# Kernel optimization log

Hardware: AMD Instinct MI355X
Metric: run time of the kernel (lower is better)

The kernel has to match this reference:

```python
import jax, jax.numpy as jnp
import numpy as np

B, S, D = 8, 1024, 768
H = 12
HD = D // H  # 64
SCALE = 1.0 / (HD ** 0.5)


def setup_inputs() -> dict:
    key = jax.random.key(0)
    ks = jax.random.split(key, 5)
    x = jax.random.normal(ks[0], (B, S, D), dtype=jnp.float32)
    W_qkv = jax.random.normal(ks[1], (D, 3 * D), dtype=jnp.float32) * 0.02
    b_qkv = jax.random.normal(ks[2], (3 * D,), dtype=jnp.float32) * 0.02
    W_proj = jax.random.normal(ks[3], (D, D), dtype=jnp.float32) * 0.02
    b_proj = jax.random.normal(ks[4], (D,), dtype=jnp.float32) * 0.02
    return {"x": x, "W_qkv": W_qkv, "b_qkv": b_qkv, "W_proj": W_proj, "b_proj": b_proj}


def reference(x, W_qkv, b_qkv, W_proj, b_proj):
    b, s, d = x.shape
    # QKV projection: (B, S, 3D) -> (3, B, H, S, HD)
    qkv = x @ W_qkv + b_qkv
    qkv = qkv.reshape(b, s, 3, H, HD).transpose(2, 0, 3, 1, 4)
    q, k, v = qkv[0], qkv[1], qkv[2]
    # scaled dot-product attention (full matrix, as in the original)
    scores = jnp.einsum("bhqd,bhkd->bhqk", q, k) * SCALE
    attn = jax.nn.softmax(scores, axis=-1)
    out = jnp.einsum("bhqk,bhkd->bhqd", attn, v)
    # merge heads: (B, S, D)
    out = out.transpose(0, 2, 1, 3).reshape(b, s, d)
    return out @ W_proj + b_proj
```

## Files before the change

### kernel.cpp

```cpp
#include <hip/hip_runtime.h>
#include <math.h>

typedef __attribute__((ext_vector_type(8))) unsigned short ushortx8;
typedef __attribute__((ext_vector_type(8))) __bf16 bf16x8;
typedef __attribute__((ext_vector_type(4))) float floatx4;
typedef __attribute__((ext_vector_type(16))) float floatx16;

#define NH 12
#define SEQ 1024
#define DM 768
#define HD 64
#define GK 768
#define QK_SCALE 0.18033688011112042f

#define GLDS16(gp, lp) __builtin_amdgcn_global_load_lds( \
    (const __attribute__((address_space(1))) unsigned int*)(const void*)(gp), \
    (__attribute__((address_space(3))) unsigned int*)(lp), 16, 0, 0)

__device__ __forceinline__ unsigned short f2bf(float f) {
    union { float f; unsigned u; } v; v.f = f;
    unsigned r = v.u + 0x7fffu + ((v.u >> 16) & 1u);
    return (unsigned short)(r >> 16);
}

__device__ __forceinline__ unsigned pk2bf(float f0, float f1) {
    union { float f; unsigned u; } a, b; a.f = f0; b.f = f1;
    return ((a.u + 0x8000u) >> 16) | ((b.u + 0x8000u) & 0xffff0000u);
}

__device__ __forceinline__ float fast_exp2(float x) {
    float r;
    asm("v_exp_f32 %0, %1" : "=v"(r) : "v"(x));
    return r;
}

__global__ void k_prep(const float* __restrict__ x, unsigned short* __restrict__ x_bf,
                       const float* __restrict__ Wqkv, unsigned short* __restrict__ WqkvT,
                       const float* __restrict__ Wproj, unsigned short* __restrict__ WprojT) {
    __shared__ float tile[32][33];
    int bx = blockIdx.x;
    if (bx < 6144) {
        int i = bx * 256 + threadIdx.x;
        float4 v = ((const float4*)x)[i];
        ushort4 o;
        o.x = f2bf(v.x); o.y = f2bf(v.y); o.z = f2bf(v.z); o.w = f2bf(v.w);
        ((ushort4*)x_bf)[i] = o;
        return;
    }
    const float* in; unsigned short* out; int R, C, c0, r0;
    if (bx < 7872) {
        int t = bx - 6144;
        in = Wqkv; out = WqkvT; R = 768; C = 2304;
        c0 = (t % 72) * 32; r0 = (t / 72) * 32;
    } else {
        int t = bx - 7872;
        in = Wproj; out = WprojT; R = 768; C = 768;
        c0 = (t % 24) * 32; r0 = (t / 24) * 32;
    }
    int tx = threadIdx.x & 31, ty = threadIdx.x >> 5;
#pragma unroll
    for (int i = 0; i < 4; i++)
        tile[ty + 8 * i][tx] = in[(size_t)(r0 + ty + 8 * i) * C + c0 + tx];
    __syncthreads();
#pragma unroll
    for (int i = 0; i < 4; i++)
        out[(size_t)(c0 + ty + 8 * i) * R + r0 + tx] = f2bf(tile[tx][ty + 8 * i]);
}

__device__ __forceinline__ void stage6(const unsigned short* gA, const unsigned short* gB,
                                       unsigned short* lbuf, int w, int k0) {
#pragma unroll
    for (int g = 0; g < 4; g++)
        GLDS16(gA + (size_t)(w * 64 + g * 16) * GK + k0, lbuf + (w * 64 + g * 16) * 32);
#pragma unroll
    for (int g = 0; g < 2; g++)
        GLDS16(gB + (size_t)(w * 32 + g * 16) * GK + k0, lbuf + 8192 + (w * 32 + g * 16) * 32);
}

__device__ __forceinline__ void mfma24(const unsigned short* Ab, const unsigned short* Bb,
                                       int wm, int wn, int l15, int csw,
                                       floatx4 (&acc)[8][3]) {
    bf16x8 af[8], bfr[3];
#pragma unroll
    for (int m = 0; m < 8; m++)
        af[m] = __builtin_bit_cast(bf16x8,
            *(const ushortx8*)&Ab[(wm * 128 + m * 16 + l15) * 32 + csw]);
#pragma unroll
    for (int n = 0; n < 3; n++)
        bfr[n] = __builtin_bit_cast(bf16x8,
            *(const ushortx8*)&Bb[(wn * 48 + n * 16 + l15) * 32 + csw]);
#pragma unroll
    for (int m = 0; m < 8; m++)
#pragma unroll
        for (int n = 0; n < 3; n++)
            acc[m][n] = __builtin_amdgcn_mfma_f32_16x16x32_bf16(af[m], bfr[n], acc[m][n], 0, 0, 0);
}

__device__ __forceinline__ void gemm_mainloop(const unsigned short* __restrict__ A,
                                              const unsigned short* __restrict__ Bt,
                                              unsigned short* smem, int m0, int n0,
                                              int w, int lane, floatx4 (&acc)[8][3]) {
    int quad = lane >> 4, l15 = lane & 15;
    int wm = w >> 1, wn = w & 1;
    int rA = lane >> 2;
    int cSwz = ((lane & 3) ^ ((lane >> 3) & 3)) * 8;
    int csw = (quad ^ ((l15 >> 1) & 3)) * 8;
    const unsigned short* gA = A + (size_t)(m0 + rA) * GK + cSwz;
    const unsigned short* gB = Bt + (size_t)(n0 + rA) * GK + cSwz;

    stage6(gA, gB, smem, w, 0);
    stage6(gA, gB, smem + 12288, w, 32);
#pragma unroll 1
    for (int t = 0; t < 24; t++) {
        if (t < 23) asm volatile("s_waitcnt vmcnt(6)" ::: "memory");
        else        asm volatile("s_waitcnt vmcnt(0)" ::: "memory");
        __builtin_amdgcn_s_barrier();
        asm volatile("" ::: "memory");
        const unsigned short* Ab = smem + (t & 1) * 12288;
        __builtin_amdgcn_s_setprio(1);
        mfma24(Ab, Ab + 8192, wm, wn, l15, csw, acc);
        __builtin_amdgcn_s_setprio(0);
        asm volatile("" ::: "memory");
        __builtin_amdgcn_s_barrier();
        asm volatile("" ::: "memory");
        if (t < 22) stage6(gA, gB, smem + (t & 1) * 12288, w, (t + 2) * 32);
    }
}

__global__ __launch_bounds__(256, 3) void k_gemm_qkv(
    const unsigned short* __restrict__ A, const unsigned short* __restrict__ Bt,
    const float* __restrict__ bias,
    unsigned short* __restrict__ Qb, unsigned short* __restrict__ Kb,
    unsigned short* __restrict__ Vt) {
    __shared__ unsigned short smem[25344];
    int tid = threadIdx.x;
    int w = tid >> 6, lane = tid & 63;
    int quad = lane >> 4, l15 = lane & 15;
    int wm = w >> 1, wn = w & 1;
    int lin = blockIdx.x;
    int xcd = lin & 7, slot = lin >> 3;
    int mt_i = xcd * 4 + (slot & 3);
    int nt_i = slot >> 2;
    int m0 = mt_i * 256, n0 = nt_i * 96;

    floatx4 acc[8][3] = {};
    gemm_mainloop(A, Bt, smem, m0, n0, w, lane, acc);

    int tsel = nt_i / 8;
    int bb = m0 >> 10;
    int s_base0 = (m0 & 1023) + wm * 128;
    if (tsel < 2) {
        unsigned short* __restrict__ dst = (tsel == 0) ? Qb : Kb;
#pragma unroll
        for (int m = 0; m < 8; m++) {
            int s_base = s_base0 + m * 16 + quad * 4;
#pragma unroll
            for (int n = 0; n < 3; n++) {
                int n_g = n0 + wn * 48 + n * 16 + l15;
                int nloc = n_g - tsel * 768;
                int hh = nloc >> 6, dd = nloc & 63;
                float bv = bias[n_g];
                size_t base = ((size_t)(bb * NH + hh) * SEQ + s_base) * HD + dd;
                if (tsel == 0) {
#pragma unroll
                    for (int rg = 0; rg < 4; rg++)
                        dst[base + (size_t)rg * HD] = f2bf((acc[m][n][rg] + bv) * QK_SCALE);
                } else {
#pragma unroll
                    for (int rg = 0; rg < 4; rg++)
                        dst[base + (size_t)rg * HD] = f2bf(acc[m][n][rg] + bv);
                }
            }
        }
    } else {
        __syncthreads();
#pragma unroll
        for (int m = 0; m < 8; m++) {
#pragma unroll
            for (int n = 0; n < 3; n++) {
                int col = wn * 48 + n * 16 + l15;
                float bv = bias[n0 + col];
                ushort4 pk;
                pk.x = f2bf(acc[m][n][0] + bv);
                pk.y = f2bf(acc[m][n][1] + bv);
                pk.z = f2bf(acc[m][n][2] + bv);
                pk.w = f2bf(acc[m][n][3] + bv);
                *(ushort4*)&smem[col * 264 + wm * 128 + m * 16 + quad * 4] = pk;
            }
        }
        __syncthreads();
        if (tid < 192) {
            int col = tid >> 1, part = tid & 1;
            int dglob = (n0 - 1536) + col;
            int hh = dglob >> 6, dd = dglob & 63;
            size_t gbase = ((size_t)(bb * NH + hh) * HD + dd) * SEQ + (m0 & 1023) + part * 128;
#pragma unroll
            for (int i = 0; i < 16; i++)
                *(uint4*)&Vt[gbase + i * 8] = *(const uint4*)&smem[col * 264 + part * 128 + i * 8];
        }
    }
}

__global__ __launch_bounds__(256) void k_attn(
    const unsigned short* __restrict__ Qb, const unsigned short* __restrict__ Kb,
    const unsigned short* __restrict__ Vt, unsigned short* __restrict__ attn_out) {
    __shared__ unsigned short smem[16384];
    unsigned short* Ks = smem;
    unsigned short* Vts = smem + 8192;
    int tid = threadIdx.x;
    int w = tid >> 6, lane = tid & 63;
    int l31 = lane & 31, lh = lane >> 5;
    int lin = blockIdx.x;
    int xcd = lin & 7, slot = lin >> 3;
    int bh = xcd * 12 + (slot >> 3);
    int qt = slot & 7;
    int b = bh / NH, h = bh - b * NH;
    const unsigned short* Qp = Qb + (size_t)bh * SEQ * HD;
    const unsigned short* Kp = Kb + (size_t)bh * SEQ * HD;
    const unsigned short* Vp = Vt + (size_t)bh * HD * SEQ;
    int q0w = qt * 128 + w * 32;

    bf16x8 qf[4];
#pragma unroll
    for (int ds = 0; ds < 4; ds++)
        qf[ds] = __builtin_bit_cast(bf16x8,
            *(const ushortx8*)&Qp[(size_t)(q0w + l31) * HD + ds * 16 + lh * 8]);

    floatx16 o[2] = {};
    float lsum = 0.f;

    int rr = tid >> 3, cc8 = (tid & 7) * 8;
    int cs = cc8 ^ ((rr & 7) * 8);
    int rsw = (l31 & 7) * 8;

    {
        uint4 a = *(const uint4*)&Kp[(size_t)rr * HD + cc8];
        uint4 b2 = *(const uint4*)&Kp[(size_t)(rr + 32) * HD + cc8];
        uint4 c = *(const uint4*)&Vp[(size_t)rr * SEQ + cc8];
        uint4 d = *(const uint4*)&Vp[(size_t)(rr + 32) * SEQ + cc8];
        *(uint4*)&Ks[rr * 64 + cs] = a;
        *(uint4*)&Ks[(rr + 32) * 64 + cs] = b2;
        *(uint4*)&Vts[rr * 64 + cs] = c;
        *(uint4*)&Vts[(rr + 32) * 64 + cs] = d;
    }
    uint4 kr0 = *(const uint4*)&Kp[(size_t)(64 + rr) * HD + cc8];
    uint4 kr1 = *(const uint4*)&Kp[(size_t)(64 + rr + 32) * HD + cc8];
    uint4 vr0 = *(const uint4*)&Vp[(size_t)rr * SEQ + 64 + cc8];
    uint4 vr1 = *(const uint4*)&Vp[(size_t)(rr + 32) * SEQ + 64 + cc8];
    __syncthreads();

    for (int kb = 0; kb < SEQ; kb += 64) {
        int cur = (kb >> 6) & 1;
        if (kb + 64 < SEQ) {
            *(uint4*)&Ks[(cur ^ 1) * 4096 + rr * 64 + cs] = kr0;
            *(uint4*)&Ks[(cur ^ 1) * 4096 + (rr + 32) * 64 + cs] = kr1;
            *(uint4*)&Vts[(cur ^ 1) * 4096 + rr * 64 + cs] = vr0;
            *(uint4*)&Vts[(cur ^ 1) * 4096 + (rr + 32) * 64 + cs] = vr1;
            if (kb + 128 < SEQ) {
                kr0 = *(const uint4*)&Kp[(size_t)(kb + 128 + rr) * HD + cc8];
                kr1 = *(const uint4*)&Kp[(size_t)(kb + 128 + rr + 32) * HD + cc8];
                vr0 = *(const uint4*)&Vp[(size_t)rr * SEQ + kb + 128 + cc8];
                vr1 = *(const uint4*)&Vp[(size_t)(rr + 32) * SEQ + kb + 128 + cc8];
            }
        }

        floatx16 sc[2] = {};
        __builtin_amdgcn_s_setprio(1);
#pragma unroll
        for (int mt = 0; mt < 2; mt++)
#pragma unroll
            for (int ds = 0; ds < 4; ds++) {
                bf16x8 kf = __builtin_bit_cast(bf16x8,
                    *(const ushortx8*)&Ks[cur * 4096 + (mt * 32 + l31) * 64 + ((ds * 16 + lh * 8) ^ rsw)]);
                sc[mt] = __builtin_amdgcn_mfma_f32_32x32x16_bf16(kf, qf[ds], sc[mt], 0, 0, 0);
            }
        __builtin_amdgcn_s_setprio(0);

        float p0[16], p1[16];
#pragma unroll
        for (int r = 0; r < 16; r++) {
            p0[r] = fast_exp2(sc[0][r]);
            p1[r] = fast_exp2(sc[1][r]);
            lsum += p0[r] + p1[r];
        }

        uint4 pw[4];
#pragma unroll
        for (int mt = 0; mt < 2; mt++) {
            const float* pp = mt ? p1 : p0;
#pragma unroll
            for (int hf = 0; hf < 2; hf++) {
                unsigned a, bq, c, d;
                asm("v_cvt_pk_bf16_f32 %0, %1, %2" : "=v"(a)  : "v"(pp[hf * 8 + 0]), "v"(pp[hf * 8 + 1]));
                asm("v_cvt_pk_bf16_f32 %0, %1, %2" : "=v"(bq) : "v"(pp[hf * 8 + 4]), "v"(pp[hf * 8 + 5]));
                asm("v_cvt_pk_bf16_f32 %0, %1, %2" : "=v"(c)  : "v"(pp[hf * 8 + 2]), "v"(pp[hf * 8 + 3]));
                asm("v_cvt_pk_bf16_f32 %0, %1, %2" : "=v"(d)  : "v"(pp[hf * 8 + 6]), "v"(pp[hf * 8 + 7]));
                asm("v_permlane32_swap_b32 %0, %1" : "+v"(a), "+v"(bq));
                asm("v_permlane32_swap_b32 %0, %1" : "+v"(c), "+v"(d));
                uint4 wv; wv.x = a; wv.y = c; wv.z = bq; wv.w = d;
                pw[mt * 2 + hf] = wv;
            }
        }

        __builtin_amdgcn_s_setprio(1);
#pragma unroll
        for (int ks = 0; ks < 4; ks++) {
            bf16x8 pf = __builtin_bit_cast(bf16x8, pw[ks]);
#pragma unroll
            for (int mt = 0; mt < 2; mt++) {
                bf16x8 vf = __builtin_bit_cast(bf16x8,
                    *(const ushortx8*)&Vts[cur * 4096 + (mt * 32 + l31) * 64 + ((ks * 16 + lh * 8) ^ rsw)]);
                o[mt] = __builtin_amdgcn_mfma_f32_32x32x16_bf16(vf, pf, o[mt], 0, 0, 0);
            }
        }
        __builtin_amdgcn_s_setprio(0);

        __syncthreads();
    }

    lsum += __shfl_xor(lsum, 32, 64);
    float inv = 1.0f / lsum;

    unsigned short* Ptw = smem + w * 2304;
#pragma unroll
    for (int mt = 0; mt < 2; mt++)
#pragma unroll
        for (int g = 0; g < 4; g++) {
            uint2 pk;
            pk.x = pk2bf(o[mt][g * 4 + 0] * inv, o[mt][g * 4 + 1] * inv);
            pk.y = pk2bf(o[mt][g * 4 + 2] * inv, o[mt][g * 4 + 3] * inv);
            *(uint2*)&Ptw[l31 * 72 + mt * 32 + g * 8 + lh * 4] = pk;
        }
    __builtin_amdgcn_s_barrier();
#pragma unroll
    for (int pass = 0; pass < 4; pass++) {
        int row = pass * 8 + (lane >> 3);
        int col8 = (lane & 7) * 8;
        uint4 vv = *(const uint4*)&Ptw[row * 72 + col8];
        *(uint4*)&attn_out[(size_t)(b * SEQ + q0w + row) * DM + h * HD + col8] = vv;
    }
}

__device__ __forceinline__ void stage4(const unsigned short* gA, const unsigned short* gB,
                                       unsigned short* lbuf, int w, int k0) {
#pragma unroll
    for (int g = 0; g < 2; g++)
        GLDS16(gA + (size_t)(w * 32 + g * 16) * GK + k0, lbuf + (w * 32 + g * 16) * 32);
#pragma unroll
    for (int g = 0; g < 2; g++)
        GLDS16(gB + (size_t)(w * 32 + g * 16) * GK + k0, lbuf + 4096 + (w * 32 + g * 16) * 32);
}

__device__ __forceinline__ void mfma12(const unsigned short* Ab, const unsigned short* Bb,
                                       int wm, int wn, int l15, int csw,
                                       floatx4 (&acc)[4][3]) {
    bf16x8 af[4], bfr[3];
#pragma unroll
    for (int m = 0; m < 4; m++)
        af[m] = __builtin_bit_cast(bf16x8,
            *(const ushortx8*)&Ab[(wm * 64 + m * 16 + l15) * 32 + csw]);
#pragma unroll
    for (int n = 0; n < 3; n++)
        bfr[n] = __builtin_bit_cast(bf16x8,
            *(const ushortx8*)&Bb[(wn * 48 + n * 16 + l15) * 32 + csw]);
#pragma unroll
    for (int m = 0; m < 4; m++)
#pragma unroll
        for (int n = 0; n < 3; n++)
            acc[m][n] = __builtin_amdgcn_mfma_f32_16x16x32_bf16(af[m], bfr[n], acc[m][n], 0, 0, 0);
}

__global__ __launch_bounds__(256, 2) void k_gemm_proj(
    const unsigned short* __restrict__ A, const unsigned short* __restrict__ Bt,
    const float* __restrict__ bias, float* __restrict__ out) {
    __shared__ unsigned short smem[16384];
    int tid = threadIdx.x;
    int w = tid >> 6, lane = tid & 63;
    int quad = lane >> 4, l15 = lane & 15;
    int wm = w >> 1, wn = w & 1;
    int lin = blockIdx.x;
    int xcd = lin & 7, slot = lin >> 3;
    int mt_i = xcd * 8 + (slot & 7);
    int nt_i = slot >> 3;
    int m0 = mt_i * 128, n0 = nt_i * 96;

    int rA = lane >> 2;
    int cSwz = ((lane & 3) ^ ((lane >> 3) & 3)) * 8;
    int csw = (quad ^ ((l15 >> 1) & 3)) * 8;
    const unsigned short* gA = A + (size_t)(m0 + rA) * GK + cSwz;
    const unsigned short* gB = Bt + (size_t)(n0 + rA) * GK + cSwz;

    floatx4 acc[4][3] = {};
    stage4(gA, gB, smem, w, 0);
    stage4(gA, gB, smem + 8192, w, 32);
#pragma unroll 1
    for (int t = 0; t < 24; t++) {
        if (t < 23) asm volatile("s_waitcnt vmcnt(4)" ::: "memory");
        else        asm volatile("s_waitcnt vmcnt(0)" ::: "memory");
        __builtin_amdgcn_s_barrier();
        asm volatile("" ::: "memory");
        const unsigned short* Ab = smem + (t & 1) * 8192;
        __builtin_amdgcn_s_setprio(1);
        mfma12(Ab, Ab + 4096, wm, wn, l15, csw, acc);
        __builtin_amdgcn_s_setprio(0);
        asm volatile("" ::: "memory");
        __builtin_amdgcn_s_barrier();
        asm volatile("" ::: "memory");
        if (t < 22) stage4(gA, gB, smem + (t & 1) * 8192, w, (t + 2) * 32);
    }

#pragma unroll
    for (int m = 0; m < 4; m++) {
        int m_base = m0 + wm * 64 + m * 16 + quad * 4;
#pragma unroll
        for (int n = 0; n < 3; n++) {
            int n_g = n0 + wn * 48 + n * 16 + l15;
            float bv = bias[n_g];
#pragma unroll
            for (int rg = 0; rg < 4; rg++)
                out[(size_t)(m_base + rg) * DM + n_g] = acc[m][n][rg] + bv;
        }
    }
}

extern "C" void kernel_launch(void* const* d_in, const int* in_sizes, int n_in,
                              void* d_out, int out_size, void* d_ws, size_t ws_size,
                              hipStream_t stream) {
    const float* x     = (const float*)d_in[0];
    const float* Wqkv  = (const float*)d_in[1];
    const float* bqkv  = (const float*)d_in[2];
    const float* Wproj = (const float*)d_in[3];
    const float* bproj = (const float*)d_in[4];
    float* out = (float*)d_out;

    char* ws = (char*)d_ws;
    unsigned short* x_bf   = (unsigned short*)(ws);
    unsigned short* WqkvT  = (unsigned short*)(ws + 12582912);
    unsigned short* WprojT = (unsigned short*)(ws + 16121856);
    unsigned short* Qb     = (unsigned short*)(ws + 17301504);
    unsigned short* Kb     = (unsigned short*)(ws + 29884416);
    unsigned short* Vt     = (unsigned short*)(ws + 42467328);
    unsigned short* attn   = (unsigned short*)(ws + 55050240);

    k_prep<<<8448, 256, 0, stream>>>(x, x_bf, Wqkv, WqkvT, Wproj, WprojT);
    k_gemm_qkv<<<768, 256, 0, stream>>>(x_bf, WqkvT, bqkv, Qb, Kb, Vt);
    k_attn<<<768, 256, 0, stream>>>(Qb, Kb, Vt, attn);
    k_gemm_proj<<<512, 256, 0, stream>>>(attn, WprojT, bproj, out);
}
```

Before: 184.5 us.

## Enlarge QKV GEMM tiles to 256x256 with 8 waves and interleaved LDS pipeline

The QKV projection GEMM moves from 256x96 tiles with 4 waves to 256x256 tiles with 8 waves and a 64-wide K step. The inner loop is split into four MFMA quarter-blocks with barriers between them, and the next global-to-LDS stage is issued before the last quarter so loads overlap compute. The larger tiles raise arithmetic intensity per LDS byte, but the grid drops to 288 blocks on a chip with many CUs, which risks under-filling the GPU. The V-transpose epilogue is redone in two halves to fit the new tile width.

```diff
diff --git a/kernel.cpp b/kernel.cpp
--- a/kernel.cpp
+++ b/kernel.cpp
@@ -67,86 +67,106 @@
         out[(size_t)(c0 + ty + 8 * i) * R + r0 + tx] = f2bf(tile[tx][ty + 8 * i]);
 }
 
-__device__ __forceinline__ void stage6(const unsigned short* gA, const unsigned short* gB,
+
+__device__ __forceinline__ void stage8(const unsigned short* gA, const unsigned short* gB,
                                        unsigned short* lbuf, int w, int k0) {
 #pragma unroll
-    for (int g = 0; g < 4; g++)
-        GLDS16(gA + (size_t)(w * 64 + g * 16) * GK + k0, lbuf + (w * 64 + g * 16) * 32);
-#pragma unroll
-    for (int g = 0; g < 2; g++)
-        GLDS16(gB + (size_t)(w * 32 + g * 16) * GK + k0, lbuf + 8192 + (w * 32 + g * 16) * 32);
-}
-
-__device__ __forceinline__ void mfma24(const unsigned short* Ab, const unsigned short* Bb,
-                                       int wm, int wn, int l15, int csw,
-                                       floatx4 (&acc)[8][3]) {
-    bf16x8 af[8], bfr[3];
-#pragma unroll
-    for (int m = 0; m < 8; m++)
-        af[m] = __builtin_bit_cast(bf16x8,
-            *(const ushortx8*)&Ab[(wm * 128 + m * 16 + l15) * 32 + csw]);
-#pragma unroll
-    for (int n = 0; n < 3; n++)
-        bfr[n] = __builtin_bit_cast(bf16x8,
-            *(const ushortx8*)&Bb[(wn * 48 + n * 16 + l15) * 32 + csw]);
-#pragma unroll
-    for (int m = 0; m < 8; m++)
-#pragma unroll
-        for (int n = 0; n < 3; n++)
-            acc[m][n] = __builtin_amdgcn_mfma_f32_16x16x32_bf16(af[m], bfr[n], acc[m][n], 0, 0, 0);
-}
-
-__device__ __forceinline__ void gemm_mainloop(const unsigned short* __restrict__ A,
-                                              const unsigned short* __restrict__ Bt,
-                                              unsigned short* smem, int m0, int n0,
-                                              int w, int lane, floatx4 (&acc)[8][3]) {
+    for (int k = 0; k < 2; k++)
+#pragma unroll
+        for (int g = 0; g < 2; g++) {
+            GLDS16(gA + (size_t)(g * 128 + w * 16) * GK + k0 + k * 32,
+                   lbuf + k * 8192 + (g * 128 + w * 16) * 32);
+            GLDS16(gB + (size_t)(g * 128 + w * 16) * GK + k0 + k * 32,
+                   lbuf + 16384 + k * 8192 + (g * 128 + w * 16) * 32);
+        }
+}
+
+__device__ __forceinline__ void ld_half_a(bf16x8 (&dst)[4][2], const unsigned short* Abuf,
+                                          int rbase, int l15, int csw) {
+#pragma unroll
+    for (int m = 0; m < 4; m++)
+#pragma unroll
+        for (int k = 0; k < 2; k++)
+            dst[m][k] = __builtin_bit_cast(bf16x8,
+                *(const ushortx8*)&Abuf[k * 8192 + (rbase + m * 16 + l15) * 32 + csw]);
+}
+
+__device__ __forceinline__ void ld_half_b(bf16x8 (&dst)[2][2], const unsigned short* Bbuf,
+                                          int rbase, int l15, int csw) {
+#pragma unroll
+    for (int n = 0; n < 2; n++)
+#pragma unroll
+        for (int k = 0; k < 2; k++)
+            dst[n][k] = __builtin_bit_cast(bf16x8,
+                *(const ushortx8*)&Bbuf[k * 8192 + (rbase + n * 16 + l15) * 32 + csw]);
+}
+
+__device__ __forceinline__ void mf16(const bf16x8 (&af)[4][2], const bf16x8 (&bf_)[2][2],
+                                     floatx4 (&acc)[8][4], int mi0, int ni0) {
+    __builtin_amdgcn_s_setprio(1);
+#pragma unroll
+    for (int m = 0; m < 4; m++)
+#pragma unroll
+        for (int n = 0; n < 2; n++)
+#pragma unroll
+            for (int k = 0; k < 2; k++)
+                acc[mi0 + m][ni0 + n] = __builtin_amdgcn_mfma_f32_16x16x32_bf16(
+                    af[m][k], bf_[n][k], acc[mi0 + m][ni0 + n], 0, 0, 0);
+    __builtin_amdgcn_s_setprio(0);
+}
+
+__global__ __launch_bounds__(512) void k_gemm_qkv(
+    const unsigned short* __restrict__ A, const unsigned short* __restrict__ Bt,
+    const float* __restrict__ bias,
+    unsigned short* __restrict__ Qb, unsigned short* __restrict__ Kb,
+    unsigned short* __restrict__ Vt) {
+    __shared__ unsigned short smem[65536];
+    int tid = threadIdx.x;
+    int w = tid >> 6, lane = tid & 63;
     int quad = lane >> 4, l15 = lane & 15;
-    int wm = w >> 1, wn = w & 1;
+    int wm = w >> 2, wn = w & 3;
+    int lin = blockIdx.x;
+    int xcd = lin & 7, slot = lin >> 3;
+    int mt_i = xcd * 4 + (slot & 3);
+    int nt_i = slot >> 2;
+    int m0 = mt_i * 256, n0 = nt_i * 256;
+
     int rA = lane >> 2;
     int cSwz = ((lane & 3) ^ ((lane >> 3) & 3)) * 8;
     int csw = (quad ^ ((l15 >> 1) & 3)) * 8;
     const unsigned short* gA = A + (size_t)(m0 + rA) * GK + cSwz;
     const unsigned short* gB = Bt + (size_t)(n0 + rA) * GK + cSwz;
 
-    stage6(gA, gB, smem, w, 0);
-    stage6(gA, gB, smem + 12288, w, 32);
+    floatx4 acc[8][4] = {};
+    stage8(gA, gB, smem, w, 0);
+    stage8(gA, gB, smem + 32768, w, 64);
 #pragma unroll 1
-    for (int t = 0; t < 24; t++) {
-        if (t < 23) asm volatile("s_waitcnt vmcnt(6)" ::: "memory");
+    for (int t = 0; t < 12; t++) {
+        if (t < 11) asm volatile("s_waitcnt vmcnt(8)" ::: "memory");
         else        asm volatile("s_waitcnt vmcnt(0)" ::: "memory");
         __builtin_amdgcn_s_barrier();
         asm volatile("" ::: "memory");
-        const unsigned short* Ab = smem + (t & 1) * 12288;
-        __builtin_amdgcn_s_setprio(1);
-        mfma24(Ab, Ab + 8192, wm, wn, l15, csw, acc);
-        __builtin_amdgcn_s_setprio(0);
-        asm volatile("" ::: "memory");
-        __builtin_amdgcn_s_barrier();
-        asm volatile("" ::: "memory");
-        if (t < 22) stage6(gA, gB, smem + (t & 1) * 12288, w, (t + 2) * 32);
-    }
-}
-
-__global__ __launch_bounds__(256, 3) void k_gemm_qkv(
-    const unsigned short* __restrict__ A, const unsigned short* __restrict__ Bt,
-    const float* __restrict__ bias,
-    unsigned short* __restrict__ Qb, unsigned short* __restrict__ Kb,
-    unsigned short* __restrict__ Vt) {
-    __shared__ unsigned short smem[25344];
-    int tid = threadIdx.x;
-    int w = tid >> 6, lane = tid & 63;
-    int quad = lane >> 4, l15 = lane & 15;
-    int wm = w >> 1, wn = w & 1;
-    int lin = blockIdx.x;
-    int xcd = lin & 7, slot = lin >> 3;
-    int mt_i = xcd * 4 + (slot & 3);
-    int nt_i = slot >> 2;
-    int m0 = mt_i * 256, n0 = nt_i * 96;
-
-    floatx4 acc[8][3] = {};
-    gemm_mainloop(A, Bt, smem, m0, n0, w, lane, acc);
-
-    int tsel = nt_i / 8;
+        unsigned short* buf = smem + (t & 1) * 32768;
+        const unsigned short* Abuf = buf;
+        const unsigned short* Bbuf = buf + 16384;
+        bf16x8 af[4][2], b0[2][2], b1[2][2];
+        ld_half_a(af, Abuf, wm * 128, l15, csw);
+        ld_half_b(b0, Bbuf, wn * 64, l15, csw);
+        mf16(af, b0, acc, 0, 0);
+        __builtin_amdgcn_s_barrier();
+        ld_half_b(b1, Bbuf, wn * 64 + 32, l15, csw);
+        mf16(af, b1, acc, 0, 2);
+        __builtin_amdgcn_s_barrier();
+        ld_half_a(af, Abuf, wm * 128 + 64, l15, csw);
+        mf16(af, b0, acc, 4, 0);
+        asm volatile("" ::: "memory");
+        __builtin_amdgcn_s_barrier();
+        asm volatile("" ::: "memory");
+        if (t < 10) stage8(gA, gB, buf, w, (t + 2) * 64);
+        mf16(af, b1, acc, 4, 2);
+    }
+
+    int tsel = nt_i / 3;
     int bb = m0 >> 10;
     int s_base0 = (m0 & 1023) + wm * 128;
     if (tsel < 2) {
@@ -155,8 +175,8 @@
         for (int m = 0; m < 8; m++) {
             int s_base = s_base0 + m * 16 + quad * 4;
 #pragma unroll
-            for (int n = 0; n < 3; n++) {
-                int n_g = n0 + wn * 48 + n * 16 + l15;
+            for (int n = 0; n < 4; n++) {
+                int n_g = n0 + wn * 64 + n * 16 + l15;
                 int nloc = n_g - tsel * 768;
                 int hh = nloc >> 6, dd = nloc & 63;
                 float bv = bias[n_g];
@@ -173,30 +193,33 @@
             }
         }
     } else {
-        __syncthreads();
-#pragma unroll
-        for (int m = 0; m < 8; m++) {
-#pragma unroll
-            for (int n = 0; n < 3; n++) {
-                int col = wn * 48 + n * 16 + l15;
-                float bv = bias[n0 + col];
-                ushort4 pk;
-                pk.x = f2bf(acc[m][n][0] + bv);
-                pk.y = f2bf(acc[m][n][1] + bv);
-                pk.z = f2bf(acc[m][n][2] + bv);
-                pk.w = f2bf(acc[m][n][3] + bv);
-                *(ushort4*)&smem[col * 264 + wm * 128 + m * 16 + quad * 4] = pk;
-            }
-        }
-        __syncthreads();
-        if (tid < 192) {
-            int col = tid >> 1, part = tid & 1;
-            int dglob = (n0 - 1536) + col;
+        int n0v = n0 - 1536;
+        for (int hf = 0; hf < 2; hf++) {
+            __syncthreads();
+            if ((wn >> 1) == hf) {
+#pragma unroll
+                for (int m = 0; m < 8; m++) {
+#pragma unroll
+                    for (int n = 0; n < 4; n++) {
+                        int colL = (wn & 1) * 64 + n * 16 + l15;
+                        float bv = bias[n0 + hf * 128 + colL];
+                        ushort4 pk;
+                        pk.x = f2bf(acc[m][n][0] + bv);
+                        pk.y = f2bf(acc[m][n][1] + bv);
+                        pk.z = f2bf(acc[m][n][2] + bv);
+                        pk.w = f2bf(acc[m][n][3] + bv);
+                        *(ushort4*)&smem[colL * 264 + wm * 128 + m * 16 + quad * 4] = pk;
+                    }
+                }
+            }
+            __syncthreads();
+            int col = tid >> 2, part = tid & 3;
+            int dglob = n0v + hf * 128 + col;
             int hh = dglob >> 6, dd = dglob & 63;
-            size_t gbase = ((size_t)(bb * NH + hh) * HD + dd) * SEQ + (m0 & 1023) + part * 128;
-#pragma unroll
-            for (int i = 0; i < 16; i++)
-                *(uint4*)&Vt[gbase + i * 8] = *(const uint4*)&smem[col * 264 + part * 128 + i * 8];
+            size_t gbase = ((size_t)(bb * NH + hh) * HD + dd) * SEQ + (m0 & 1023) + part * 64;
+#pragma unroll
+            for (int i = 0; i < 8; i++)
+                *(uint4*)&Vt[gbase + i * 8] = *(const uint4*)&smem[col * 264 + part * 64 + i * 8];
         }
     }
 }
@@ -443,7 +466,7 @@
     unsigned short* attn   = (unsigned short*)(ws + 55050240);
 
     k_prep<<<8448, 256, 0, stream>>>(x, x_bf, Wqkv, WqkvT, Wproj, WprojT);
-    k_gemm_qkv<<<768, 256, 0, stream>>>(x_bf, WqkvT, bqkv, Qb, Kb, Vt);
+    k_gemm_qkv<<<288, 512, 0, stream>>>(x_bf, WqkvT, bqkv, Qb, Kb, Vt);
     k_attn<<<768, 256, 0, stream>>>(Qb, Kb, Vt, attn);
     k_gemm_proj<<<512, 256, 0, stream>>>(attn, WprojT, bproj, out);
 }
```

Result: slower. 208.0 us (+12.7%).
